# Optimization experiments

Measured on AMD Instinct MI355X. Metric: run time of the kernel, lower is better.

The kernel has to match this reference:

```python
import jax, jax.numpy as jnp
import numpy as np
import math

F_FEATS = 51
BATCH = 256
N_WINDOW = 10
W_IN = N_WINDOW - 1          # input_window = 9
BUCKET = 6
EMB = 6
HEADS = 3
DHEAD = EMB // HEADS
FFN = 12
TOP_M = 80
HID = F_FEATS * EMB          # 306


def _layernorm(x, s, b, eps=1e-5):
    mu = jnp.mean(x, -1, keepdims=True)
    var = jnp.var(x, -1, keepdims=True)
    return (x - mu) / jnp.sqrt(var + eps) * s + b


def setup_inputs() -> dict:
    key = jax.random.key(0)
    ks = jax.random.split(key, 32)
    g = lambda i, shape, sc=0.1: jax.random.normal(ks[i], shape, dtype=jnp.float32) * sc
    inp = {
        "src": jax.random.uniform(ks[0], (N_WINDOW, BATCH, F_FEATS), dtype=jnp.float32),
        "tgt": jax.random.uniform(ks[1], (N_WINDOW, BATCH, F_FEATS), dtype=jnp.float32),
        # AutoDis params, batched over features (torch loops over n_feats modules)
        "w1_w": g(2, (F_FEATS, BUCKET), 0.5),          # Linear(1,bs) weight squeezed
        "w1_b": g(3, (F_FEATS, BUCKET)),
        "w2_w": g(4, (F_FEATS, BUCKET, BUCKET), 0.3),  # torch layout (out,in)
        "w2_b": g(5, (F_FEATS, BUCKET)),
        "meta": g(6, (F_FEATS, BUCKET, EMB), 0.5),     # EmbeddingBag table per feature
        # Sparse top-m MHSA (1 layer, post-norm encoder)
        "Wq": g(7, (EMB, EMB), 0.3), "bq": g(8, (EMB,)),
        "Wk": g(9, (EMB, EMB), 0.3), "bk": g(10, (EMB,)),
        "Wv": g(11, (EMB, EMB), 0.3), "bv": g(12, (EMB,)),
        "Wo": g(13, (EMB, EMB), 0.3), "bo": g(14, (EMB,)),
        "ln1_s": jnp.ones((EMB,), jnp.float32), "ln1_b": jnp.zeros((EMB,), jnp.float32),
        "ffn_w1": g(15, (FFN, EMB), 0.3), "ffn_b1": g(16, (FFN,)),
        "ffn_w2": g(17, (EMB, FFN), 0.3), "ffn_b2": g(18, (EMB,)),
        "ln2_s": jnp.ones((EMB,), jnp.float32), "ln2_b": jnp.zeros((EMB,), jnp.float32),
        # GRU (1 layer), torch gate order r,z,n
        "gru_wih": g(19, (3 * HID, HID), 0.05),
        "gru_whh": g(20, (3 * HID, HID), 0.05),
        "gru_bih": g(21, (3 * HID,)),
        "gru_bhh": g(22, (3 * HID,)),
        "h0": g(23, (1, BATCH, HID), 1.0),             # init_hidden
        # final FCN
        "fcn_w": g(24, (F_FEATS, HID), 0.05),
        "fcn_b": g(25, (F_FEATS,)),
    }
    return inp


def reference(src, tgt, w1_w, w1_b, w2_w, w2_b, meta,
              Wq, bq, Wk, bk, Wv, bv, Wo, bo,
              ln1_s, ln1_b, ffn_w1, ffn_b1, ffn_w2, ffn_b2, ln2_s, ln2_b,
              gru_wih, gru_whh, gru_bih, gru_bhh, h0, fcn_w, fcn_b):
    s = src[:-1]                                  # [W=9, B, F]
    W, B, F = s.shape
    # ---- AutoDis, vectorized across all features (replaces per-feature loop) ----
    h1 = jax.nn.leaky_relu(s[..., None] * w1_w + w1_b)            # [W,B,F,6]
    h2 = jnp.einsum('wbfi,fji->wbfj', h1, w2_w) + w2_b            # Linear(bs,bs)
    probs = jax.nn.softmax((h2 + 0.5 * h1) / 1e-5, axis=-1)      # temperature 1e-5
    emb = jnp.einsum('wbfi,fie->wbfe', probs, meta)               # weighted EmbeddingBag sum
    # rearrange 'w b f e -> b (w f) e' and scale by sqrt(emb)
    x = emb.transpose(1, 0, 2, 3).reshape(B, W * F, EMB) * math.sqrt(EMB)
    # ---- Sparse top-m MHSA encoder layer (post-norm) ----
    T = W * F                                                     # 459 tokens
    def heads(t):
        return t.reshape(B, T, HEADS, DHEAD).transpose(0, 2, 1, 3)
    q = heads(x @ Wq.T + bq)
    k = heads(x @ Wk.T + bk)
    v = heads(x @ Wv.T + bv)
    scores = jnp.einsum('bhqd,bhkd->bhqk', q, k) / math.sqrt(DHEAD)
    kth = jax.lax.top_k(scores, TOP_M)[0][..., -1:]               # m-th largest per query
    scores = jnp.where(scores >= kth, scores, -jnp.inf)           # keep only top-m keys
    attn = jax.nn.softmax(scores, axis=-1)
    o = jnp.einsum('bhqk,bhkd->bhqd', attn, v).transpose(0, 2, 1, 3).reshape(B, T, EMB)
    x = _layernorm(x + (o @ Wo.T + bo), ln1_s, ln1_b)
    f = jax.nn.relu(x @ ffn_w1.T + ffn_b1) @ ffn_w2.T + ffn_b2
    x = _layernorm(x + f, ln2_s, ln2_b)
    # rearrange 'b (w f) e -> w b (f e)'
    seq = x.reshape(B, W, F, EMB).transpose(1, 0, 2, 3).reshape(W, B, F * EMB)
    # ---- GRU over seq[:-1] (8 steps) ----
    def step(h, xt):
        gi = xt @ gru_wih.T + gru_bih
        gh = h @ gru_whh.T + gru_bhh
        ir, iz, inn = jnp.split(gi, 3, -1)
        hr, hz, hn = jnp.split(gh, 3, -1)
        r = jax.nn.sigmoid(ir + hr)
        z = jax.nn.sigmoid(iz + hz)
        n = jnp.tanh(inn + r * hn)
        h = (1.0 - z) * n + z * h
        return h, None
    hT, _ = jax.lax.scan(step, h0[0, :B], seq[:-1])               # lstm_out[-1] == final hidden
    out = jax.nn.sigmoid(hT @ fcn_w.T + fcn_b)[None]              # [1, B, F]
    return out


if __name__ == '__main__':
    o = reference(**setup_inputs())
    print(o.shape)
```

## Files before the change

kernel.cpp:

```cpp
#include <hip/hip_runtime.h>
#include <math.h>

#define WWIN 9
#define BATCH 256
#define FEAT 51
#define TT 459
#define EMBD 6
#define HID 306
#define G3 918
#define FFND 12
#define TOPM 80
#define MAXTASK 320
#define NPAIR 153
#define WSTRIDE 920

__device__ __forceinline__ float leakyf(float v){ return v >= 0.f ? v : 0.01f*v; }
__device__ __forceinline__ float sigmf(float v){ return 1.f/(1.f+__expf(-v)); }

__device__ __forceinline__ unsigned fkey(float s){
    unsigned fb = __float_as_uint(s);
    unsigned m = (unsigned)((int)fb >> 31);
    return fb ^ (m | 0x80000000u);
}
__device__ __forceinline__ float fkey_inv(unsigned k){
    unsigned fb = (k & 0x80000000u) ? (k ^ 0x80000000u) : ~k;
    return __uint_as_float(fb);
}
__device__ __forceinline__ unsigned bfrne(float f){
    unsigned u = __float_as_uint(f);
    u += 0x7fffu + ((u >> 16) & 1u);
    return u >> 16;
}

template<int CTRL, int RMASK>
__device__ __forceinline__ float dpp_add(float v){
    int r = __builtin_amdgcn_update_dpp(0, __float_as_int(v), CTRL, RMASK, 0xf, true);
    return v + __int_as_float(r);
}
__device__ __forceinline__ float wave_fsum(float v){
    v = dpp_add<0x111, 0xf>(v);
    v = dpp_add<0x112, 0xf>(v);
    v = dpp_add<0x114, 0xf>(v);
    v = dpp_add<0x118, 0xf>(v);
    v = dpp_add<0x142, 0xa>(v);
    v = dpp_add<0x143, 0xc>(v);
    return __int_as_float(__builtin_amdgcn_readlane(__float_as_int(v), 63));
}
template<int CTRL, int RMASK>
__device__ __forceinline__ unsigned dpp_uadd(unsigned v){
    unsigned r = (unsigned)__builtin_amdgcn_update_dpp(0, (int)v, CTRL, RMASK, 0xf, true);
    return v + r;
}
__device__ __forceinline__ unsigned wave_usum(unsigned v){
    v = dpp_uadd<0x111, 0xf>(v);
    v = dpp_uadd<0x112, 0xf>(v);
    v = dpp_uadd<0x114, 0xf>(v);
    v = dpp_uadd<0x118, 0xf>(v);
    v = dpp_uadd<0x142, 0xa>(v);
    v = dpp_uadd<0x143, 0xc>(v);
    return (unsigned)__builtin_amdgcn_readlane((int)v, 63);
}
template<int CTRL, int RMASK>
__device__ __forceinline__ unsigned dpp_min(unsigned v){
    unsigned r = (unsigned)__builtin_amdgcn_update_dpp((int)v, (int)v, CTRL, RMASK, 0xf, false);
    return v < r ? v : r;
}
__device__ __forceinline__ unsigned wave_umin(unsigned v){
    v = dpp_min<0x111, 0xf>(v);
    v = dpp_min<0x112, 0xf>(v);
    v = dpp_min<0x114, 0xf>(v);
    v = dpp_min<0x118, 0xf>(v);
    v = dpp_min<0x142, 0xa>(v);
    v = dpp_min<0x143, 0xc>(v);
    return (unsigned)__builtin_amdgcn_readlane((int)v, 63);
}

__global__ __launch_bounds__(512) void embed_tasks(
    const float* __restrict__ src,
    const float* __restrict__ w1w, const float* __restrict__ w1b,
    const float* __restrict__ w2w, const float* __restrict__ w2b,
    const float* __restrict__ meta,
    const float* __restrict__ Wq, const float* __restrict__ bq,
    const float* __restrict__ Wk, const float* __restrict__ bk,
    const float* __restrict__ Wv, const float* __restrict__ bv,
    const float* __restrict__ wih, const float* __restrict__ whh,
    const float* __restrict__ fcw,
    float* __restrict__ WIHT, unsigned* __restrict__ WHB, float* __restrict__ FCNT,
    float* __restrict__ X, float* __restrict__ Q,
    float* __restrict__ K, float* __restrict__ V,
    int* __restrict__ TASKS, int* __restrict__ ROWMAP, int* __restrict__ NT)
{
    __shared__ int sbuck[TT];
    int b = blockIdx.x;
    int t = threadIdx.x;

    for (int idx = blockIdx.x*512 + threadIdx.x; idx < G3*HID; idx += 256*512){
        int o = idx / HID, i = idx % HID;
        WIHT[i*G3 + o] = wih[idx];
    }
    for (int idx = blockIdx.x*512 + threadIdx.x; idx < NPAIR*WSTRIDE; idx += 256*512){
        int p = idx / WSTRIDE, c = idx % WSTRIDE;
        unsigned v = 0u;
        if (c < G3){
            unsigned lo = bfrne(whh[(size_t)c*HID + 2*p]);
            unsigned hi = bfrne(whh[(size_t)c*HID + 2*p + 1]);
            v = lo | (hi << 16);
        }
        WHB[idx] = v;
    }
    for (int idx = blockIdx.x*512 + threadIdx.x; idx < FEAT*HID; idx += 256*512){
        int f = idx / HID, i = idx % HID;
        FCNT[i*FEAT + f] = fcw[idx];
    }

    if (t < TT){
        int w = t / FEAT, f = t % FEAT;
        float s = src[(w*BATCH + b)*FEAT + f];
        float h1[EMBD], h2[EMBD];
        #pragma unroll
        for (int i=0;i<EMBD;i++) h1[i] = leakyf(s*w1w[f*EMBD+i] + w1b[f*EMBD+i]);
        #pragma unroll
        for (int j=0;j<EMBD;j++){
            float a = 0.f;
            #pragma unroll
            for (int i=0;i<EMBD;i++) a += h1[i]*w2w[(f*EMBD+j)*EMBD+i];
            h2[j] = a + w2b[f*EMBD+j];
        }
        float z[EMBD];
        float m = -INFINITY; int jm = 0;
        #pragma unroll
        for (int j=0;j<EMBD;j++){
            z[j] = (h2[j] + 0.5f*h1[j]) * 1e+05f;
            if (z[j] > m){ m = z[j]; jm = j; }
        }
        float se = 0.f;
        #pragma unroll
        for (int j=0;j<EMBD;j++){ z[j] = expf(z[j]-m); se += z[j]; }
        float inv = 1.0f / se;
        #pragma unroll
        for (int j=0;j<EMBD;j++) z[j] *= inv;
        sbuck[t] = jm;

        float xr[EMBD];
        #pragma unroll
        for (int e=0;e<EMBD;e++){
            float a = 0.f;
            #pragma unroll
            for (int i=0;i<EMBD;i++) a += z[i]*meta[(f*EMBD+i)*EMBD+e];
            xr[e] = a * 2.449489742783178f;
        }
        float* xp = X + (b*TT + t)*EMBD;
        float* qp = Q + (b*TT + t)*EMBD;
        float* kp = K + (b*TT + t)*EMBD;
        float* vp = V + (b*TT + t)*EMBD;
        #pragma unroll
        for (int e=0;e<EMBD;e++){
            xp[e] = xr[e];
            float aq=0.f, ak=0.f, av=0.f;
            #pragma unroll
            for (int i=0;i<EMBD;i++){
                aq += xr[i]*Wq[e*EMBD+i];
                ak += xr[i]*Wk[e*EMBD+i];
                av += xr[i]*Wv[e*EMBD+i];
            }
            qp[e] = aq + bq[e];
            kp[e] = ak + bk[e];
            vp[e] = av + bv[e];
        }
    }
    __syncthreads();
    if (threadIdx.x < 64){
        int f = threadIdx.x;
        unsigned mask = 0; unsigned cnts = 0; int repw[6]; int cnt = 0;
        if (f < FEAT){
            #pragma unroll
            for (int w=0; w<WWIN; w++){
                int j = sbuck[w*FEAT + f];
                if (!((mask>>j) & 1u)){ mask |= 1u<<j; repw[j] = w; }
                cnts += 1u << (5*j);
            }
            cnt = __popc(mask);
        }
        int inc = cnt;
        #pragma unroll
        for (int off=1; off<64; off<<=1){
            int n = __shfl_up(inc, off, 64);
            if (threadIdx.x >= off) inc += n;
        }
        int offset = inc - cnt;
        if (f < FEAT){
            int rk = 0;
            #pragma unroll
            for (int j=0;j<6;j++){
                if ((mask>>j) & 1u){
                    int mult = (int)((cnts >> (5*j)) & 31u);
                    TASKS[b*MAXTASK + offset + rk] =
                        (mult<<13) | (f<<7) | (j<<4) | repw[j];
                    rk++;
                }
            }
            #pragma unroll
            for (int w=0;w<WWIN;w++){
                int j = sbuck[w*FEAT + f];
                int r = __popc(mask & ((1u<<j)-1u));
                ROWMAP[b*TT + w*FEAT + f] = offset + r;
            }
        }
        if (threadIdx.x == 63) NT[b] = inc;
    }
}

__global__ __launch_bounds__(256) void attn_topk(
    const float* __restrict__ Q, const float* __restrict__ K,
    const float* __restrict__ V, const int* __restrict__ TASKS,
    const int* __restrict__ NT, float2* __restrict__ OD)
{
    int blk = blockIdx.x;
    int b = blk / 3, h = blk % 3;
    const int base = b*TT*EMBD + 2*h;
    int wave = threadIdx.x >> 6, lane = threadIdx.x & 63;
    int nt = NT[b];

    float rkx[4], rky[4], rvx[4], rvy[4], rmf[4];
    unsigned rpm[4];
    #pragma unroll
    for (int s=0;s<4;s++){
        int tix = lane + (s<<6);
        rkx[s]=0.f; rky[s]=0.f; rvx[s]=0.f; rvy[s]=0.f; rmf[s]=0.f; rpm[s]=0u;
        if (tix < nt){
            int pk = TASKS[b*MAXTASK + tix];
            int rep_t = (pk & 15)*FEAT + ((pk >> 7) & 63);
            int mult = pk >> 13;
            rkx[s] = K[base + rep_t*EMBD];
            rky[s] = K[base + rep_t*EMBD + 1];
            rvx[s] = V[base + rep_t*EMBD];
            rvy[s] = V[base + rep_t*EMBD + 1];
            rmf[s] = (float)mult;
            rpm[s] = ((unsigned)mult << 10) | 1u;
        }
    }

    const float SC = 0.7071067811865476f;
    for (int idx = blockIdx.y*4 + wave; idx < nt; idx += 16){
        int pk = TASKS[b*MAXTASK + idx];
        int rep_t = (pk & 15)*FEAT + ((pk >> 7) & 63);
        float q0 = Q[base + rep_t*EMBD]     * SC;
        float q1 = Q[base + rep_t*EMBD + 1] * SC;

        float sv[4]; unsigned uk[4];
        #pragma unroll
        for (int s=0;s<4;s++){
            float sc = q0*rkx[s] + q1*rky[s];
            sv[s] = sc;
            uk[s] = rpm[s] ? fkey(sc) : 0u;
        }
        unsigned T = 0;
        int Dwin = nt, Dabove = 0;
        int mode = 0; unsigned Ue = 0;
        for (int bit = 31; bit >= 0; --bit){
            unsigned Tp = T | (1u<<bit);
            unsigned acc = 0;
            #pragma unroll
            for (int s=0;s<4;s++) acc += (uk[s] >= Tp) ? rpm[s] : 0u;
            acc = wave_usum(acc);
            int cw = (int)(acc >> 10);
            int dg = (int)(acc & 1023u);
            int dhi = dg - Dabove;
            if (cw >= TOPM){
                T = Tp; Dwin = dhi;
                if (cw == TOPM){ mode = 1; break; }
            } else {
                Dwin -= dhi; Dabove = dg;
            }
            if (Dwin == 1){ mode = 2; Ue = T + (1u<<bit); break; }
        }
        if (mode == 0)      Ue = T + 1u;
        else if (mode == 1) Ue = 0xFFFFFFFFu;
        unsigned mn = 0xFFFFFFFFu;
        #pragma unroll
        for (int s=0;s<4;s++){
            unsigned cand = (rpm[s] && uk[s] >= T && uk[s] < Ue) ? uk[s] : 0xFFFFFFFFu;
            mn = min(mn, cand);
        }
        unsigned kth = wave_umin(mn);
        float skth = fkey_inv(kth);
        float den=0.f, ox=0.f, oy=0.f;
        #pragma unroll
        for (int s=0;s<4;s++){
            float p = __expf(sv[s] - skth) * rmf[s];
            p = (uk[s] >= kth) ? p : 0.f;
            den += p; ox += p*rvx[s]; oy += p*rvy[s];
        }
        den = wave_fsum(den);
        ox  = wave_fsum(ox);
        oy  = wave_fsum(oy);
        if (lane == 0){
            float id = 1.0f/den;
            OD[(b*3 + h)*MAXTASK + idx] = make_float2(ox*id, oy*id);
        }
    }
}

__global__ __launch_bounds__(256) void post_gi(
    const float* __restrict__ X, const float2* __restrict__ OD,
    const int* __restrict__ ROWMAP,
    const float* __restrict__ Wo, const float* __restrict__ bo,
    const float* __restrict__ l1s, const float* __restrict__ l1b,
    const float* __restrict__ fw1, const float* __restrict__ fb1,
    const float* __restrict__ fw2, const float* __restrict__ fb2,
    const float* __restrict__ l2s, const float* __restrict__ l2b,
    const float* __restrict__ WIHT, const float* __restrict__ bih,
    float* __restrict__ GI)
{
    __shared__ float sL[8][HID];
    int gy = blockIdx.y, gx = blockIdx.x;
    for (int idx = threadIdx.x; idx < 8*FEAT; idx += 256){
        int k = idx / FEAT, ff = idx % FEAT;
        int r = gy*8 + k;
        int w = r >> 8, b = r & 255;
        int t = w*FEAT + ff;
        const float* xr = X + (b*TT + t)*EMBD;
        int rm = ROWMAP[b*TT + t];
        float orow[EMBD];
        #pragma unroll
        for (int h=0;h<3;h++){
            float2 od = OD[(b*3 + h)*MAXTASK + rm];
            orow[2*h]   = od.x;
            orow[2*h+1] = od.y;
        }
        float y[EMBD];
        #pragma unroll
        for (int e=0;e<EMBD;e++){
            float a = 0.f;
            #pragma unroll
            for (int e2=0;e2<EMBD;e2++) a += orow[e2]*Wo[e*EMBD+e2];
            y[e] = xr[e] + a + bo[e];
        }
        float mu=0.f;
        #pragma unroll
        for (int e=0;e<EMBD;e++) mu += y[e];
        mu *= (1.f/6.f);
        float var=0.f;
        #pragma unroll
        for (int e=0;e<EMBD;e++){ float d = y[e]-mu; var += d*d; }
        var *= (1.f/6.f);
        float isd = 1.0f / sqrtf(var + 1e-05f);
        float xn[EMBD];
        #pragma unroll
        for (int e=0;e<EMBD;e++) xn[e] = (y[e]-mu)*isd*l1s[e] + l1b[e];
        float hd[FFND];
        #pragma unroll
        for (int kk2=0;kk2<FFND;kk2++){
            float a = fb1[kk2];
            #pragma unroll
            for (int e=0;e<EMBD;e++) a += xn[e]*fw1[kk2*EMBD+e];
            hd[kk2] = fmaxf(a, 0.f);
        }
        float y2[EMBD];
        #pragma unroll
        for (int e=0;e<EMBD;e++){
            float a = fb2[e];
            #pragma unroll
            for (int kk2=0;kk2<FFND;kk2++) a += hd[kk2]*fw2[e*FFND+kk2];
            y2[e] = xn[e] + a;
        }
        float mu2=0.f;
        #pragma unroll
        for (int e=0;e<EMBD;e++) mu2 += y2[e];
        mu2 *= (1.f/6.f);
        float var2=0.f;
        #pragma unroll
        for (int e=0;e<EMBD;e++){ float d = y2[e]-mu2; var2 += d*d; }
        var2 *= (1.f/6.f);
        float isd2 = 1.0f / sqrtf(var2 + 1e-05f);
        #pragma unroll
        for (int e=0;e<EMBD;e++) sL[k][ff*EMBD+e] = (y2[e]-mu2)*isd2*l2s[e] + l2b[e];
    }
    __syncthreads();
    int col = gx*256 + threadIdx.x;
    if (col >= G3) return;
    float acc[8];
    #pragma unroll
    for (int k=0;k<8;k++) acc[k] = 0.f;
    for (int i=0;i<HID;i++){
        float wv = WIHT[i*G3 + col];
        #pragma unroll
        for (int k=0;k<8;k++) acc[k] += sL[k][i]*wv;
    }
    float bb = bih[col];
    #pragma unroll
    for (int k=0;k<8;k++) GI[(size_t)(gy*8+k)*G3 + col] = acc[k] + bb;
}

#define PFP 9

#define LOADP(buf, c_) { \
    int p0_ = (c_)*PFP; \
    _Pragma("unroll") \
    for (int r=0;r<PFP;r++){ \
        const unsigned* wp = WHB + (size_t)(p0_+r)*WSTRIDE + jc; \
        buf[3*r] = wp[0]; buf[3*r+1] = wp[HID]; buf[3*r+2] = wp[2*HID]; \
    } }

#define COMPP(buf, c_) { \
    int p0_ = (c_)*PFP; \
    _Pragma("unroll") \
    for (int r=0;r<PFP;r++){ \
        float2 h2 = *(const float2*)&hL[2*(p0_+r)]; \
        unsigned pr_ = buf[3*r], pz_ = buf[3*r+1], pn_ = buf[3*r+2]; \
        float wr0 = __uint_as_float(pr_ << 16), wr1 = __uint_as_float(pr_ & 0xffff0000u); \
        float wz0 = __uint_as_float(pz_ << 16), wz1 = __uint_as_float(pz_ & 0xffff0000u); \
        float wn0 = __uint_as_float(pn_ << 16), wn1 = __uint_as_float(pn_ & 0xffff0000u); \
        ar = fmaf(wr0, h2.x, fmaf(wr1, h2.y, ar)); \
        az = fmaf(wz0, h2.x, fmaf(wz1, h2.y, az)); \
        an = fmaf(wn0, h2.x, fmaf(wn1, h2.y, an)); \
    } }

__global__ __launch_bounds__(320) void gru_fcn(
    const float* __restrict__ GI, const unsigned* __restrict__ WHB,
    const float* __restrict__ bhh, const float* __restrict__ h0,
    const float* __restrict__ FCNT, const float* __restrict__ fcb,
    float* __restrict__ out)
{
    __shared__ float hL[HID + 2];
    int b = blockIdx.x;
    int tid = threadIdx.x;
    if (tid < HID) hL[tid] = h0[(size_t)b*HID + tid];
    if (tid >= HID && tid < HID+2) hL[tid] = 0.f;
    __syncthreads();

    int j = tid;
    bool act = (j < HID);
    int jc = act ? j : 0;
    float br = bhh[jc], bz = bhh[HID+jc], bn = bhh[2*HID+jc];

    for (int step = 0; step < 8; ++step){
        const float* gi = GI + ((size_t)step*BATCH + b)*G3;
        float gr = gi[jc], gz = gi[HID+jc], gn = gi[2*HID+jc];
        float ar = 0.f, az = 0.f, an = 0.f;
        unsigned bufA[3*PFP], bufB[3*PFP];
        LOADP(bufA, 0);
        #pragma unroll 1
        for (int p = 0; p < 8; ++p){
            LOADP(bufB, 2*p+1);
            COMPP(bufA, 2*p);
            LOADP(bufA, 2*p+2);
            COMPP(bufB, 2*p+1);
        }
        COMPP(bufA, 16);
        float hold = hL[jc];
        __syncthreads();
        if (act){
            float rr = sigmf(gr + ar + br);
            float zz = sigmf(gz + az + bz);
            float nn = tanhf(gn + rr*(an + bn));
            hL[j] = (1.f - zz)*nn + zz*hold;
        }
        __syncthreads();
    }

    if (tid < FEAT){
        int f = tid;
        float acc = 0.f;
        #pragma unroll 6
        for (int i=0;i<HID;i++) acc += hL[i]*FCNT[i*FEAT+f];
        out[(size_t)b*FEAT + f] = sigmf(acc + fcb[f]);
    }
}

extern "C" void kernel_launch(void* const* d_in, const int* in_sizes, int n_in,
                              void* d_out, int out_size, void* d_ws, size_t ws_size,
                              hipStream_t stream)
{
    const float* src = (const float*)d_in[0];
    const float* w1w = (const float*)d_in[2];
    const float* w1b = (const float*)d_in[3];
    const float* w2w = (const float*)d_in[4];
    const float* w2b = (const float*)d_in[5];
    const float* meta= (const float*)d_in[6];
    const float* Wq = (const float*)d_in[7];  const float* bq = (const float*)d_in[8];
    const float* Wk = (const float*)d_in[9];  const float* bk = (const float*)d_in[10];
    const float* Wv = (const float*)d_in[11]; const float* bv = (const float*)d_in[12];
    const float* Wo = (const float*)d_in[13]; const float* bo = (const float*)d_in[14];
    const float* l1s= (const float*)d_in[15]; const float* l1b= (const float*)d_in[16];
    const float* fw1= (const float*)d_in[17]; const float* fb1= (const float*)d_in[18];
    const float* fw2= (const float*)d_in[19]; const float* fb2= (const float*)d_in[20];
    const float* l2s= (const float*)d_in[21]; const float* l2b= (const float*)d_in[22];
    const float* wih= (const float*)d_in[23]; const float* whh= (const float*)d_in[24];
    const float* bih= (const float*)d_in[25]; const float* bhh= (const float*)d_in[26];
    const float* h0 = (const float*)d_in[27];
    const float* fcw= (const float*)d_in[28]; const float* fcb= (const float*)d_in[29];

    float* ws = (float*)d_ws;
    float* X    = ws;
    float* Q    = X    + 705024;
    float* K    = Q    + 705024;
    float* V    = K    + 705024;
    float* GI   = V    + 705024;
    float* WIHT = GI   + 1880064;
    unsigned* WHB = (unsigned*)(WIHT + 280908);
    float* FCNT = (float*)(WHB + 140760);
    float* ODf  = FCNT + 15606;
    int*   TASKS= (int*)(ODf + 491520);
    int*   RMAP = TASKS + 81920;
    int*   NT   = RMAP + 117504;
    float2* OD  = (float2*)ODf;
    float* outp = (float*)d_out;

    embed_tasks<<<256, 512, 0, stream>>>(src, w1w, w1b, w2w, w2b, meta,
                                         Wq,bq,Wk,bk,Wv,bv, wih, whh, fcw,
                                         WIHT, WHB, FCNT,
                                         X,Q,K,V, TASKS, RMAP, NT);
    {
        dim3 g(768, 4);
        attn_topk<<<g, 256, 0, stream>>>(Q, K, V, TASKS, NT, OD);
    }
    {
        dim3 g(4, 256);
        post_gi<<<g, 256, 0, stream>>>(X, OD, RMAP, Wo, bo, l1s, l1b,
                                       fw1, fb1, fw2, fb2, l2s, l2b,
                                       WIHT, bih, GI);
    }
    gru_fcn<<<256, 320, 0, stream>>>(GI, WHB, bhh, h0, FCNT, fcb, outp);
}
```

Before: 204.9 us.

## Split GRU hidden matvec reduction across two thread halves per block

```diff
diff --git a/kernel.cpp b/kernel.cpp
--- a/kernel.cpp
+++ b/kernel.cpp
@@ -12,6 +12,7 @@
 #define TOPM 80
 #define MAXTASK 320
 #define NPAIR 153
+#define NPAIR2 154
 #define WSTRIDE 920
 
 __device__ __forceinline__ float leakyf(float v){ return v >= 0.f ? v : 0.01f*v; }
@@ -98,10 +99,10 @@
         int o = idx / HID, i = idx % HID;
         WIHT[i*G3 + o] = wih[idx];
     }
-    for (int idx = blockIdx.x*512 + threadIdx.x; idx < NPAIR*WSTRIDE; idx += 256*512){
+    for (int idx = blockIdx.x*512 + threadIdx.x; idx < NPAIR2*WSTRIDE; idx += 256*512){
         int p = idx / WSTRIDE, c = idx % WSTRIDE;
         unsigned v = 0u;
-        if (c < G3){
+        if (c < G3 && p < NPAIR){
             unsigned lo = bfrne(whh[(size_t)c*HID + 2*p]);
             unsigned hi = bfrne(whh[(size_t)c*HID + 2*p + 1]);
             v = lo | (hi << 16);
@@ -392,20 +393,20 @@
     for (int k=0;k<8;k++) GI[(size_t)(gy*8+k)*G3 + col] = acc[k] + bb;
 }
 
-#define PFP 9
-
-#define LOADP(buf, c_) { \
-    int p0_ = (c_)*PFP; \
+#define PFQ 7
+
+#define LOADQ(buf, c_) { \
+    int p0_ = pbase + (c_)*PFQ; \
     _Pragma("unroll") \
-    for (int r=0;r<PFP;r++){ \
+    for (int r=0;r<PFQ;r++){ \
         const unsigned* wp = WHB + (size_t)(p0_+r)*WSTRIDE + jc; \
         buf[3*r] = wp[0]; buf[3*r+1] = wp[HID]; buf[3*r+2] = wp[2*HID]; \
     } }
 
-#define COMPP(buf, c_) { \
-    int p0_ = (c_)*PFP; \
+#define COMPQ(buf, c_) { \
+    int p0_ = pbase + (c_)*PFQ; \
     _Pragma("unroll") \
-    for (int r=0;r<PFP;r++){ \
+    for (int r=0;r<PFQ;r++){ \
         float2 h2 = *(const float2*)&hL[2*(p0_+r)]; \
         unsigned pr_ = buf[3*r], pz_ = buf[3*r+1], pn_ = buf[3*r+2]; \
         float wr0 = __uint_as_float(pr_ << 16), wr1 = __uint_as_float(pr_ & 0xffff0000u); \
@@ -416,44 +417,53 @@
         an = fmaf(wn0, h2.x, fmaf(wn1, h2.y, an)); \
     } }
 
-__global__ __launch_bounds__(320) void gru_fcn(
+__global__ __launch_bounds__(640) void gru_fcn(
     const float* __restrict__ GI, const unsigned* __restrict__ WHB,
     const float* __restrict__ bhh, const float* __restrict__ h0,
     const float* __restrict__ FCNT, const float* __restrict__ fcb,
     float* __restrict__ out)
 {
     __shared__ float hL[HID + 2];
+    __shared__ float pB[HID][3];
     int b = blockIdx.x;
     int tid = threadIdx.x;
     if (tid < HID) hL[tid] = h0[(size_t)b*HID + tid];
     if (tid >= HID && tid < HID+2) hL[tid] = 0.f;
     __syncthreads();
 
-    int j = tid;
+    bool low = (tid < 320);
+    int j = low ? tid : (tid - 320);
     bool act = (j < HID);
     int jc = act ? j : 0;
-    float br = bhh[jc], bz = bhh[HID+jc], bn = bhh[2*HID+jc];
+    int pbase = low ? 0 : 77;
+    float br=0.f, bz=0.f, bn=0.f;
+    if (low && act){ br = bhh[j]; bz = bhh[HID+j]; bn = bhh[2*HID+j]; }
 
     for (int step = 0; step < 8; ++step){
-        const float* gi = GI + ((size_t)step*BATCH + b)*G3;
-        float gr = gi[jc], gz = gi[HID+jc], gn = gi[2*HID+jc];
+        float gr=0.f, gz=0.f, gn=0.f;
+        if (low && act){
+            const float* gi = GI + ((size_t)step*BATCH + b)*G3;
+            gr = gi[j]; gz = gi[HID+j]; gn = gi[2*HID+j];
+        }
         float ar = 0.f, az = 0.f, an = 0.f;
-        unsigned bufA[3*PFP], bufB[3*PFP];
-        LOADP(bufA, 0);
+        unsigned bufA[3*PFQ], bufB[3*PFQ];
+        LOADQ(bufA, 0);
         #pragma unroll 1
-        for (int p = 0; p < 8; ++p){
-            LOADP(bufB, 2*p+1);
-            COMPP(bufA, 2*p);
-            LOADP(bufA, 2*p+2);
-            COMPP(bufB, 2*p+1);
-        }
-        COMPP(bufA, 16);
-        float hold = hL[jc];
+        for (int p = 0; p < 5; ++p){
+            LOADQ(bufB, 2*p+1);
+            COMPQ(bufA, 2*p);
+            LOADQ(bufA, 2*p+2);
+            COMPQ(bufB, 2*p+1);
+        }
+        COMPQ(bufA, 10);
+        float hold = low ? hL[jc] : 0.f;
+        if (!low && act){ pB[j][0] = ar; pB[j][1] = az; pB[j][2] = an; }
         __syncthreads();
-        if (act){
-            float rr = sigmf(gr + ar + br);
-            float zz = sigmf(gz + az + bz);
-            float nn = tanhf(gn + rr*(an + bn));
+        if (low && act){
+            float anf = an + pB[j][2] + bn;
+            float rr = sigmf(gr + ar + pB[j][0] + br);
+            float zz = sigmf(gz + az + pB[j][1] + bz);
+            float nn = tanhf(gn + rr*anf);
             hL[j] = (1.f - zz)*nn + zz*hold;
         }
         __syncthreads();
@@ -499,7 +509,7 @@
     float* GI   = V    + 705024;
     float* WIHT = GI   + 1880064;
     unsigned* WHB = (unsigned*)(WIHT + 280908);
-    float* FCNT = (float*)(WHB + 140760);
+    float* FCNT = (float*)(WHB + 141680);
     float* ODf  = FCNT + 15606;
     int*   TASKS= (int*)(ODf + 491520);
     int*   RMAP = TASKS + 81920;
@@ -521,5 +531,5 @@
                                        fw1, fb1, fw2, fb2, l2s, l2b,
                                        WIHT, bih, GI);
     }
-    gru_fcn<<<256, 320, 0, stream>>>(GI, WHB, bhh, h0, FCNT, fcb, outp);
-}
+    gru_fcn<<<256, 640, 0, stream>>>(GI, WHB, bhh, h0, FCNT, fcb, outp);
+}
```

Result: faster. 191.2 us (-6.7%).
